# Kernel tuning notes

Hardware: AMD Instinct MI355X
Metric: run time of the kernel (lower is better)

## Reference

```python
import jax, jax.numpy as jnp
import numpy as np

HID = 256; NH = 8; DH = 32; NL = 2
NV = 20000; NT = 50000; NE = 100000; NC = 8; FIN = 64


def setup_inputs() -> dict:
    ks = jax.random.split(jax.random.key(0), 32)
    f = lambda i, sh, s: jax.random.normal(ks[i], sh, dtype=jnp.float32) * s
    return {
        "x_v": f(0, (NV, FIN), 1.0),
        "x_t": f(1, (NT, FIN), 1.0),
        "ei_vt_src": jax.random.randint(ks[2], (NE,), 0, NV),
        "ei_vt_dst": jax.random.randint(ks[3], (NE,), 0, NT),
        "ei_tv_src": jax.random.randint(ks[4], (NE,), 0, NT),
        "ei_tv_dst": jax.random.randint(ks[5], (NE,), 0, NV),
        "ei_tt_src": jax.random.randint(ks[6], (NE,), 0, NT),
        "ei_tt_dst": jax.random.randint(ks[7], (NE,), 0, NT),
        "current": jax.random.randint(ks[8], (NC, 2), 0, NV),
        "W_in_v": f(9, (FIN, HID), 0.05), "b_in_v": jnp.zeros((HID,)),
        "W_in_t": f(10, (FIN, HID), 0.05), "b_in_t": jnp.zeros((HID,)),
        "Wk": f(11, (NL, 2, HID, HID), 0.05), "bk": jnp.zeros((NL, 2, HID)),
        "Wq": f(12, (NL, 2, HID, HID), 0.05), "bq": jnp.zeros((NL, 2, HID)),
        "Wv": f(13, (NL, 2, HID, HID), 0.05), "bv": jnp.zeros((NL, 2, HID)),
        "Wa": f(14, (NL, 2, HID, HID), 0.05), "ba": jnp.zeros((NL, 2, HID)),
        "skip": jnp.zeros((NL, 2)),
        "a_rel": f(15, (NL, 3, NH, DH, DH), 0.1),
        "m_rel": f(16, (NL, 3, NH, DH, DH), 0.1),
        "p_rel": jnp.ones((NL, 3, NH)),
        "Ws1": f(17, (2 * HID, HID), 0.05), "bs1": jnp.zeros((HID,)),
        "Ws2": f(18, (HID, 2), 0.05), "bs2": jnp.zeros((2,)),
    }


def reference(x_v, x_t, ei_vt_src, ei_vt_dst, ei_tv_src, ei_tv_dst,
              ei_tt_src, ei_tt_dst, current,
              W_in_v, b_in_v, W_in_t, b_in_t,
              Wk, bk, Wq, bq, Wv, bv, Wa, ba, skip,
              a_rel, m_rel, p_rel, Ws1, bs1, Ws2, bs2):
    scale = 1.0 / jnp.sqrt(jnp.float32(DH))
    # input projections + relu (lin_dict)
    hv = jax.nn.relu(x_v @ W_in_v + b_in_v)
    ht = jax.nn.relu(x_t @ W_in_t + b_in_t)
    # edge types: (src_type, dst_type, rel_idx, src_idx, dst_idx); 0=vehicle, 1=track
    edges = [(0, 1, 0, ei_vt_src, ei_vt_dst),
             (1, 0, 1, ei_tv_src, ei_tv_dst),
             (1, 1, 2, ei_tt_src, ei_tt_dst)]
    for l in range(NL):
        h = (hv, ht)
        proj = lambda W, b, t: (h[t] @ W[l, t] + b[l, t]).reshape(-1, NH, DH)
        k = (proj(Wk, bk, 0), proj(Wk, bk, 1))
        q = (proj(Wq, bq, 0), proj(Wq, bq, 1))
        v = (proj(Wv, bv, 0), proj(Wv, bv, 1))
        agg = [jnp.zeros((NV, NH, DH), jnp.float32),
               jnp.zeros((NT, NH, DH), jnp.float32)]
        for (st, dt, r, si, di) in edges:
            nd = agg[dt].shape[0]
            ke = jnp.einsum('ehd,hdf->ehf', k[st][si], a_rel[l, r])  # [E,H,D]
            ve = jnp.einsum('ehd,hdf->ehf', v[st][si], m_rel[l, r])  # [E,H,D]
            logit = (q[dt][di] * ke).sum(-1) * p_rel[l, r] * scale    # [E,H]
            m = jax.ops.segment_max(logit, di, num_segments=nd)
            e = jnp.exp(logit - m[di])
            s = jax.ops.segment_sum(e, di, num_segments=nd)
            alpha = e / (s[di] + 1e-16)
            agg[dt] = agg[dt] + jax.ops.segment_sum(alpha[..., None] * ve, di,
                                                    num_segments=nd)
        new = []
        for t in (0, 1):
            o = jax.nn.gelu(agg[t].reshape(-1, HID), approximate=False) @ Wa[l, t] + ba[l, t]
            beta = jax.nn.sigmoid(skip[l, t])
            new.append(beta * o + (1.0 - beta) * h[t])
        hv, ht = new
    # batched Scorer over (current vehicles) x (all tracks); cat([track, vehicle])
    veh = hv[current[:, 0]]                 # [C,HID]
    tpart = ht @ Ws1[:HID]                  # [NT,HID]
    vpart = veh @ Ws1[HID:] + bs1           # [C,HID]
    hmid = jax.nn.relu(tpart[None, :, :] + vpart[:, None, :])  # [C,NT,HID]
    out = hmid @ Ws2 + bs2                  # [C,NT,2]
    return out[..., 0], jax.nn.sigmoid(out[..., 1])
```

## Files before the change

### kernel.cpp

```cpp
#include <hip/hip_runtime.h>
#include <hip/hip_bf16.h>
#include <math.h>

#define HID 256
#define NH 8
#define DH 32
#define NL 2
#define NV 20000
#define NT 50000
#define NE 100000
#define NC 8
#define FIN 64

typedef unsigned short u16;
typedef unsigned int u32;
typedef short s16x8 __attribute__((ext_vector_type(8)));
typedef float f32x4 __attribute__((ext_vector_type(4)));

__device__ __forceinline__ float bf2f(u16 u) { return __uint_as_float(((u32)u) << 16); }
__device__ __forceinline__ u16 f2bf(float f) {
    u32 x = __float_as_uint(f);
    u32 r = ((x >> 16) & 1u) + 0x7fffu;
    return (u16)((x + r) >> 16);
}
__device__ __forceinline__ void up2(u32 u, float& a, float& b) {
    a = __uint_as_float(u << 16);
    b = __uint_as_float(u & 0xffff0000u);
}
__device__ __forceinline__ s16x8 gelu8(s16x8 a) {
    s16x8 r;
#pragma unroll
    for (int i = 0; i < 8; i++) {
        float v = bf2f((u16)a[i]);
        v = 0.5f * v * (1.f + erff(v * 0.70710678118654752f));
        r[i] = (short)f2bf(v);
    }
    return r;
}

__global__ void k_zero_i(int* __restrict__ p, int n) {
    for (int i = blockIdx.x * 256 + threadIdx.x; i < n; i += gridDim.x * 256) p[i] = 0;
}

__global__ void k_hist3(const int* __restrict__ d0, const int* __restrict__ d1, const int* __restrict__ d2,
                        int* __restrict__ cnt3) {
    int r = blockIdx.x >> 9;
    int b = blockIdx.x & 511;
    const int* dst = (r == 0) ? d0 : (r == 1) ? d1 : d2;
    int* cnt = cnt3 + (size_t)r * NT;
    for (int e = b * 256 + threadIdx.x; e < NE; e += 512 * 256)
        atomicAdd(&cnt[dst[e]], 1);
}

__global__ __launch_bounds__(1024) void k_scan3(const int* __restrict__ cnt3,
                                                int* __restrict__ rp0, int* __restrict__ rp1, int* __restrict__ rp2) {
    int r = blockIdx.x;
    const int* cnt = cnt3 + (size_t)r * NT;
    int* rp = (r == 0) ? rp0 : (r == 1) ? rp1 : rp2;
    int n = (r == 1) ? NV : NT;
    __shared__ int wsum[16];
    __shared__ int carry_s;
    int t = threadIdx.x, lane = t & 63, wv = t >> 6;
    if (t == 0) { carry_s = 0; rp[0] = 0; }
    __syncthreads();
    for (int base = 0; base < n; base += 1024) {
        int v = (base + t < n) ? cnt[base + t] : 0;
        int x = v;
#pragma unroll
        for (int off = 1; off < 64; off <<= 1) {
            int y = __shfl_up(x, off, 64);
            if (lane >= off) x += y;
        }
        if (lane == 63) wsum[wv] = x;
        __syncthreads();
        if (wv == 0 && lane < 16) {
            int s = wsum[lane];
#pragma unroll
            for (int off = 1; off < 16; off <<= 1) {
                int y = __shfl_up(s, off, 64);
                if (lane >= off) s += y;
            }
            wsum[lane] = s;
        }
        __syncthreads();
        int prefix = carry_s + (wv > 0 ? wsum[wv - 1] : 0);
        if (base + t < n) rp[base + t + 1] = prefix + x;
        __syncthreads();
        if (t == 0) carry_s += wsum[15];
        __syncthreads();
    }
}

__global__ void k_copy3(const int* __restrict__ rp0, const int* __restrict__ rp1, const int* __restrict__ rp2,
                        int* __restrict__ fill3) {
    int r = blockIdx.x >> 8;
    int b = blockIdx.x & 255;
    const int* rp = (r == 0) ? rp0 : (r == 1) ? rp1 : rp2;
    int n = (r == 1) ? NV : NT;
    int* fill = fill3 + (size_t)r * NT;
    for (int i = b * 256 + threadIdx.x; i < n; i += 256 * 256) fill[i] = rp[i];
}

__global__ void k_scatter3(const int* __restrict__ d0, const int* __restrict__ s0,
                           const int* __restrict__ d1, const int* __restrict__ s1,
                           const int* __restrict__ d2, const int* __restrict__ s2,
                           int* __restrict__ fill3,
                           int* __restrict__ es0, int* __restrict__ es1, int* __restrict__ es2) {
    int r = blockIdx.x >> 9;
    int b = blockIdx.x & 511;
    const int* dst = (r == 0) ? d0 : (r == 1) ? d1 : d2;
    const int* src = (r == 0) ? s0 : (r == 1) ? s1 : s2;
    int* fill = fill3 + (size_t)r * NT;
    int* es = (r == 0) ? es0 : (r == 1) ? es1 : es2;
    for (int e = b * 256 + threadIdx.x; e < NE; e += 512 * 256) {
        int d = dst[e];
        int p = atomicAdd(&fill[d], 1);
        es[p] = src[e];
    }
}

__global__ __launch_bounds__(256) void k_in_proj(const float* __restrict__ X, const float* __restrict__ W,
                          const float* __restrict__ b, u16* __restrict__ Y, int N) {
    const int NPB = 16;
    __shared__ float xs[NPB][FIN];
    int n0 = blockIdx.x * NPB;
    int t = threadIdx.x;
    for (int idx = t; idx < NPB * FIN; idx += 256) {
        int i = idx >> 6, c = idx & 63;
        int n = n0 + i;
        xs[i][c] = (n < N) ? X[(size_t)n * FIN + c] : 0.f;
    }
    __syncthreads();
    float acc[NPB];
#pragma unroll
    for (int i = 0; i < NPB; i++) acc[i] = 0.f;
    for (int c = 0; c < FIN; c++) {
        float w = W[c * HID + t];
#pragma unroll
        for (int i = 0; i < NPB; i++) acc[i] += xs[i][c] * w;
    }
    float bb = b[t];
    for (int i = 0; i < NPB; i++) {
        int n = n0 + i;
        if (n < N) Y[(size_t)n * HID + t] = f2bf(fmaxf(acc[i] + bb, 0.f));
    }
}

__device__ __forceinline__ int swz_idx(int k, int n) {
    int ks = k >> 5, r = k & 31;
    int j = r & 7;
    int l = ((r >> 3) << 4) | (n & 15);
    int nt = n >> 4;
    return ((ks * 16 + nt) * 64 + l) * 8 + j;
}

__global__ __launch_bounds__(256) void k_fuse_w2(
        const float* __restrict__ Wk_, const float* __restrict__ bk_, const float* __restrict__ Rk,
        u16* __restrict__ WswK, float* __restrict__ bkO,
        const float* __restrict__ Wv_, const float* __restrict__ bv_, const float* __restrict__ Rv,
        u16* __restrict__ WswV, float* __restrict__ bvO) {
    int h = blockIdx.x & 7;
    int which = blockIdx.x >> 3;
    const float* W = which ? Wv_ : Wk_;
    const float* b = which ? bv_ : bk_;
    const float* R = which ? Rv : Rk;
    u16* Wsw = which ? WswV : WswK;
    float* bout = which ? bvO : bkO;
    __shared__ float sR[DH * DH];
    int t = threadIdx.x;
    for (int idx = t; idx < DH * DH; idx += 256) sR[idx] = R[h * DH * DH + idx];
    __syncthreads();
    int f = t & 31, c0 = t >> 5;
    for (int c = c0; c < HID; c += 8) {
        float acc = 0.f;
#pragma unroll
        for (int d = 0; d < DH; d++) acc += W[c * HID + h * DH + d] * sR[d * DH + f];
        Wsw[swz_idx(c, h * DH + f)] = f2bf(acc);
    }
    if (t < DH) {
        float acc = 0.f;
#pragma unroll
        for (int d = 0; d < DH; d++) acc += b[h * DH + d] * sR[d * DH + t];
        bout[h * DH + t] = acc;
    }
}

__global__ __launch_bounds__(256) void k_swz_multi(const float* __restrict__ Wq, const float* __restrict__ Wa,
                                                   const float* __restrict__ Ws1, u16* __restrict__ out) {
    int slot = blockIdx.x >> 8;
    int idx = ((blockIdx.x & 255) << 8) | threadIdx.x;
    const float* src = (slot < 4) ? (Wq + (size_t)slot * 65536)
                     : (slot < 8) ? (Wa + (size_t)(slot - 4) * 65536)
                                  : Ws1;
    int j = idx & 7, l = (idx >> 3) & 63, nt = (idx >> 9) & 15, ks = idx >> 13;
    int k = ks * 32 + (l >> 4) * 8 + j;
    int n = nt * 16 + (l & 15);
    out[(size_t)slot * 65536 + idx] = f2bf(src[k * HID + n]);
}

template <int MODE, int GELU>
__global__ __launch_bounds__(256) void k_mm(const u16* __restrict__ X, const u16* __restrict__ Wsw,
                                            const float* __restrict__ bias, void* __restrict__ Y,
                                            const float* __restrict__ skip_, int N) {
    int tid = threadIdx.x;
    int w = tid >> 6, lane = tid & 63;
    int r0 = blockIdx.x * 16;
    int rA = r0 + (lane & 15);
    int koffg = lane >> 4;
    s16x8 a[8];
    if (rA < N) {
        const s16x8* ap = (const s16x8*)(X + (size_t)rA * HID) + koffg;
#pragma unroll
        for (int ks = 0; ks < 8; ks++) a[ks] = ap[ks * 4];
    } else {
#pragma unroll
        for (int ks = 0; ks < 8; ks++) a[ks] = (s16x8){0, 0, 0, 0, 0, 0, 0, 0};
    }
    if (GELU) {
#pragma unroll
        for (int ks = 0; ks < 8; ks++) a[ks] = gelu8(a[ks]);
    }
    f32x4 acc[4];
#pragma unroll
    for (int nt = 0; nt < 4; nt++) acc[nt] = (f32x4){0.f, 0.f, 0.f, 0.f};
    const s16x8* wp = (const s16x8*)Wsw;
#pragma unroll
    for (int ks = 0; ks < 8; ks++) {
        const s16x8* wq = wp + (size_t)ks * 16 * 64 + lane;
#pragma unroll
        for (int nt = 0; nt < 4; nt++) {
            s16x8 b = wq[(w * 4 + nt) * 64];
            acc[nt] = __builtin_amdgcn_mfma_f32_16x16x32_bf16(a[ks], b, acc[nt], 0, 0, 0);
        }
    }
    int colb = lane & 15;
    int rowb = r0 + koffg * 4;
    float beta = 0.f, ombeta = 0.f;
    if (MODE == 2) { beta = 1.f / (1.f + expf(-skip_[0])); ombeta = 1.f - beta; }
#pragma unroll
    for (int nt = 0; nt < 4; nt++) {
        int col = w * 64 + nt * 16 + colb;
        float bb = (MODE == 1 || MODE == 3) ? 0.f : bias[col];
#pragma unroll
        for (int j = 0; j < 4; j++) {
            int row = rowb + j;
            if (row < N) {
                float v = acc[nt][j] + bb;
                if (MODE == 0 || MODE == 3) {
                    ((u16*)Y)[(size_t)row * HID + col] = f2bf(v);
                } else if (MODE == 1) {
                    ((float*)Y)[(size_t)row * HID + col] = v;
                } else {
                    u16* hp = (u16*)Y + (size_t)row * HID + col;
                    *hp = f2bf(beta * v + ombeta * bf2f(*hp));
                }
            }
        }
    }
}

__global__ __launch_bounds__(256) void k_mm_gt(const u16* __restrict__ agg, const u16* __restrict__ WaSw,
                                               const float* __restrict__ ba_, const float* __restrict__ skip_,
                                               const u16* __restrict__ ht_old, const u16* __restrict__ Ws1Sw,
                                               u16* __restrict__ tpart, int N) {
    __shared__ u16 sH[16][264];
    int tid = threadIdx.x;
    int w = tid >> 6, lane = tid & 63;
    int r0 = blockIdx.x * 16;
    int rA = r0 + (lane & 15);
    int koffg = lane >> 4;
    s16x8 a[8];
    {
        const s16x8* ap = (const s16x8*)(agg + (size_t)rA * HID) + koffg;
#pragma unroll
        for (int ks = 0; ks < 8; ks++) a[ks] = gelu8(ap[ks * 4]);
    }
    f32x4 acc[4];
#pragma unroll
    for (int nt = 0; nt < 4; nt++) acc[nt] = (f32x4){0.f, 0.f, 0.f, 0.f};
    const s16x8* wp = (const s16x8*)WaSw;
#pragma unroll
    for (int ks = 0; ks < 8; ks++) {
        const s16x8* wq = wp + (size_t)ks * 16 * 64 + lane;
#pragma unroll
        for (int nt = 0; nt < 4; nt++)
            acc[nt] = __builtin_amdgcn_mfma_f32_16x16x32_bf16(a[ks], wq[(w * 4 + nt) * 64], acc[nt], 0, 0, 0);
    }
    float beta = 1.f / (1.f + expf(-skip_[0])), ombeta = 1.f - beta;
    int colb = lane & 15;
    int rowl = koffg * 4;
#pragma unroll
    for (int nt = 0; nt < 4; nt++) {
        int col = w * 64 + nt * 16 + colb;
        float bb = ba_[col];
#pragma unroll
        for (int j = 0; j < 4; j++) {
            int row = r0 + rowl + j;
            float v = acc[nt][j] + bb;
            float o = beta * v + ombeta * bf2f(ht_old[(size_t)row * HID + col]);
            sH[rowl + j][col] = f2bf(o);
        }
    }
    __syncthreads();
    s16x8 a2[8];
#pragma unroll
    for (int ks = 0; ks < 8; ks++)
        a2[ks] = *(const s16x8*)&sH[lane & 15][ks * 32 + koffg * 8];
#pragma unroll
    for (int nt = 0; nt < 4; nt++) acc[nt] = (f32x4){0.f, 0.f, 0.f, 0.f};
    const s16x8* wp2 = (const s16x8*)Ws1Sw;
#pragma unroll
    for (int ks = 0; ks < 8; ks++) {
        const s16x8* wq = wp2 + (size_t)ks * 16 * 64 + lane;
#pragma unroll
        for (int nt = 0; nt < 4; nt++)
            acc[nt] = __builtin_amdgcn_mfma_f32_16x16x32_bf16(a2[ks], wq[(w * 4 + nt) * 64], acc[nt], 0, 0, 0);
    }
#pragma unroll
    for (int nt = 0; nt < 4; nt++) {
        int col = w * 64 + nt * 16 + colb;
#pragma unroll
        for (int j = 0; j < 4; j++) {
            int row = r0 + rowl + j;
            if (row < N) tpart[(size_t)row * HID + col] = f2bf(acc[nt][j]);
        }
    }
}

__global__ __launch_bounds__(256) void k_mm2(const u16* __restrict__ X,
                                             const u16* __restrict__ W1, const float* __restrict__ b1, u16* __restrict__ Y1,
                                             const u16* __restrict__ W2, const float* __restrict__ b2, u16* __restrict__ Y2,
                                             int N) {
    int tid = threadIdx.x;
    int w = tid >> 6, lane = tid & 63;
    int r0 = blockIdx.x * 16;
    int rA = r0 + (lane & 15);
    int koffg = lane >> 4;
    s16x8 a[8];
    if (rA < N) {
        const s16x8* ap = (const s16x8*)(X + (size_t)rA * HID) + koffg;
#pragma unroll
        for (int ks = 0; ks < 8; ks++) a[ks] = ap[ks * 4];
    } else {
#pragma unroll
        for (int ks = 0; ks < 8; ks++) a[ks] = (s16x8){0, 0, 0, 0, 0, 0, 0, 0};
    }
    int colb = lane & 15;
    int rowb = r0 + koffg * 4;
#pragma unroll
    for (int pass = 0; pass < 2; pass++) {
        const u16* Wsw = pass ? W2 : W1;
        const float* bias = pass ? b2 : b1;
        u16* Y = pass ? Y2 : Y1;
        f32x4 acc[4];
#pragma unroll
        for (int nt = 0; nt < 4; nt++) acc[nt] = (f32x4){0.f, 0.f, 0.f, 0.f};
        const s16x8* wp = (const s16x8*)Wsw;
#pragma unroll
        for (int ks = 0; ks < 8; ks++) {
            const s16x8* wq = wp + (size_t)ks * 16 * 64 + lane;
#pragma unroll
            for (int nt = 0; nt < 4; nt++) {
                s16x8 b = wq[(w * 4 + nt) * 64];
                acc[nt] = __builtin_amdgcn_mfma_f32_16x16x32_bf16(a[ks], b, acc[nt], 0, 0, 0);
            }
        }
#pragma unroll
        for (int nt = 0; nt < 4; nt++) {
            int col = w * 64 + nt * 16 + colb;
            float bb = bias[col];
#pragma unroll
            for (int j = 0; j < 4; j++) {
                int row = rowb + j;
                if (row < N) Y[(size_t)row * HID + col] = f2bf(acc[nt][j] + bb);
            }
        }
    }
}

__global__ __launch_bounds__(256) void k_mm3(const u16* __restrict__ X,
                                             const u16* __restrict__ W0, const float* __restrict__ b0, u16* __restrict__ Y0,
                                             const u16* __restrict__ W1, const float* __restrict__ b1, u16* __restrict__ Y1,
                                             const u16* __restrict__ W2, const float* __restrict__ b2, u16* __restrict__ Y2,
                                             int N) {
    int tid = threadIdx.x;
    int w = tid >> 6, lane = tid & 63;
    int r0 = blockIdx.x * 16;
    int rA = r0 + (lane & 15);
    int koffg = lane >> 4;
    s16x8 a[8];
    if (rA < N) {
        const s16x8* ap = (const s16x8*)(X + (size_t)rA * HID) + koffg;
#pragma unroll
        for (int ks = 0; ks < 8; ks++) a[ks] = ap[ks * 4];
    } else {
#pragma unroll
        for (int ks = 0; ks < 8; ks++) a[ks] = (s16x8){0, 0, 0, 0, 0, 0, 0, 0};
    }
    int colb = lane & 15;
    int rowb = r0 + koffg * 4;
#pragma unroll
    for (int pass = 0; pass < 3; pass++) {
        const u16* Wsw = (pass == 0) ? W0 : (pass == 1) ? W1 : W2;
        const float* bias = (pass == 0) ? b0 : (pass == 1) ? b1 : b2;
        u16* Y = (pass == 0) ? Y0 : (pass == 1) ? Y1 : Y2;
        f32x4 acc[4];
#pragma unroll
        for (int nt = 0; nt < 4; nt++) acc[nt] = (f32x4){0.f, 0.f, 0.f, 0.f};
        const s16x8* wp = (const s16x8*)Wsw;
#pragma unroll
        for (int ks = 0; ks < 8; ks++) {
            const s16x8* wq = wp + (size_t)ks * 16 * 64 + lane;
#pragma unroll
            for (int nt = 0; nt < 4; nt++) {
                s16x8 b = wq[(w * 4 + nt) * 64];
                acc[nt] = __builtin_amdgcn_mfma_f32_16x16x32_bf16(a[ks], b, acc[nt], 0, 0, 0);
            }
        }
#pragma unroll
        for (int nt = 0; nt < 4; nt++) {
            int col = w * 64 + nt * 16 + colb;
            float bb = bias[col];
#pragma unroll
            for (int j = 0; j < 4; j++) {
                int row = rowb + j;
                if (row < N) Y[(size_t)row * HID + col] = f2bf(acc[nt][j] + bb);
            }
        }
    }
}

__device__ __forceinline__ void attn_pass(const u16* __restrict__ kA, const u16* __restrict__ vM,
                                          const int* __restrict__ es, int jb, int je,
                                          float q0, float q1, float q2, float q3, float ph, int lane4,
                                          float& o0, float& o1, float& o2, float& o3) {
    float m = -INFINITY, ss = 0.f, a0 = 0.f, a1 = 0.f, a2 = 0.f, a3 = 0.f;
    uint2 ku0 = {0, 0}, vu0 = {0, 0}, ku1 = {0, 0}, vu1 = {0, 0};
    if (jb < je) {
        int s = es[jb];
        ku0 = *(const uint2*)(kA + (size_t)s * HID + lane4);
        vu0 = *(const uint2*)(vM + (size_t)s * HID + lane4);
    }
    if (jb + 1 < je) {
        int s = es[jb + 1];
        ku1 = *(const uint2*)(kA + (size_t)s * HID + lane4);
        vu1 = *(const uint2*)(vM + (size_t)s * HID + lane4);
    }
    for (int j = jb; j < je; j++) {
        uint2 ku = ku0, vu = vu0;
        ku0 = ku1; vu0 = vu1;
        if (j + 2 < je) {
            int s = es[j + 2];
            ku1 = *(const uint2*)(kA + (size_t)s * HID + lane4);
            vu1 = *(const uint2*)(vM + (size_t)s * HID + lane4);
        }
        float k0, k1, k2, k3; up2(ku.x, k0, k1); up2(ku.y, k2, k3);
        float part = q0 * k0 + q1 * k1 + q2 * k2 + q3 * k3;
        part += __shfl_xor(part, 1, 64);
        part += __shfl_xor(part, 2, 64);
        part += __shfl_xor(part, 4, 64);
        float logit = part * ph;
        float nm = fmaxf(m, logit);
        float corr = expf(m - nm);
        float ee = expf(logit - nm);
        float v0, v1, v2, v3; up2(vu.x, v0, v1); up2(vu.y, v2, v3);
        ss = ss * corr + ee;
        a0 = a0 * corr + ee * v0; a1 = a1 * corr + ee * v1;
        a2 = a2 * corr + ee * v2; a3 = a3 * corr + ee * v3;
        m = nm;
    }
    float inv = 1.f / (ss + 1e-16f);
    o0 += a0 * inv; o1 += a1 * inv; o2 += a2 * inv; o3 += a3 * inv;
}

__global__ __launch_bounds__(256) void k_node_attn(
        const u16* __restrict__ q, const u16* __restrict__ kA, const u16* __restrict__ vM,
        const int* __restrict__ rp, const int* __restrict__ es,
        const float* __restrict__ P, float scale,
        u16* __restrict__ agg, int Nd) {
    int node = blockIdx.x * 4 + (threadIdx.x >> 6);
    if (node >= Nd) return;
    int lane = threadIdx.x & 63;
    float ph = P[lane >> 3] * scale;
    uint2 qu = *(const uint2*)(q + (size_t)node * HID + lane * 4);
    float q0, q1, q2, q3; up2(qu.x, q0, q1); up2(qu.y, q2, q3);
    float o0 = 0.f, o1 = 0.f, o2 = 0.f, o3 = 0.f;
    attn_pass(kA, vM, es, rp[node], rp[node + 1], q0, q1, q2, q3, ph, lane * 4, o0, o1, o2, o3);
    u16* ap = agg + (size_t)node * HID + lane * 4;
    ap[0] = f2bf(o0); ap[1] = f2bf(o1); ap[2] = f2bf(o2); ap[3] = f2bf(o3);
}

__global__ __launch_bounds__(256) void k_node_attn2(
        const u16* __restrict__ q,
        const u16* __restrict__ kA0, const u16* __restrict__ vM0,
        const int* __restrict__ rp0, const int* __restrict__ es0, const float* __restrict__ P0,
        const u16* __restrict__ kA1, const u16* __restrict__ vM1,
        const int* __restrict__ rp1, const int* __restrict__ es1, const float* __restrict__ P1,
        float scale, u16* __restrict__ agg, int Nd) {
    int node = blockIdx.x * 4 + (threadIdx.x >> 6);
    if (node >= Nd) return;
    int lane = threadIdx.x & 63;
    int h = lane >> 3;
    int lane4 = lane * 4;
    float ph0 = P0[h] * scale, ph1 = P1[h] * scale;
    uint2 qu = *(const uint2*)(q + (size_t)node * HID + lane4);
    float q0, q1, q2, q3; up2(qu.x, q0, q1); up2(qu.y, q2, q3);
    float o0 = 0.f, o1 = 0.f, o2 = 0.f, o3 = 0.f;
    attn_pass(kA0, vM0, es0, rp0[node], rp0[node + 1], q0, q1, q2, q3, ph0, lane4, o0, o1, o2, o3);
    attn_pass(kA1, vM1, es1, rp1[node], rp1[node + 1], q0, q1, q2, q3, ph1, lane4, o0, o1, o2, o3);
    u16* ap = agg + (size_t)node * HID + lane4;
    ap[0] = f2bf(o0); ap[1] = f2bf(o1); ap[2] = f2bf(o2); ap[3] = f2bf(o3);
}

__global__ void k_vpart(const u16* __restrict__ hv, const int* __restrict__ current,
                        const float* __restrict__ Ws1, const float* __restrict__ bs1,
                        float* __restrict__ vpart) {
    __shared__ float row[HID];
    int t = threadIdx.x;
    for (int c = 0; c < NC; c++) {
        int n = current[c * 2];
        row[t] = bf2f(hv[(size_t)n * HID + t]);
        __syncthreads();
        float acc = 0.f;
        for (int i = 0; i < HID; i++) acc += row[i] * Ws1[(size_t)(HID + i) * HID + t];
        vpart[c * HID + t] = acc + bs1[t];
        __syncthreads();
    }
}

__global__ __launch_bounds__(256) void k_final(const u16* __restrict__ tpart, const float* __restrict__ vpart,
                        const float* __restrict__ Ws2, const float* __restrict__ bs2,
                        float* __restrict__ out) {
    __shared__ float vp[NC * HID];
    int t = threadIdx.x;
    for (int idx = t; idx < NC * HID; idx += 256) vp[idx] = vpart[idx];
    __syncthreads();
    int lane = t & 63, w = t >> 6;
    float w20[4], w21[4];
#pragma unroll
    for (int i = 0; i < 4; i++) {
        w20[i] = Ws2[(lane + 64 * i) * 2 + 0];
        w21[i] = Ws2[(lane + 64 * i) * 2 + 1];
    }
    float b0 = bs2[0], b1 = bs2[1];
    for (int n = blockIdx.x * 4 + w; n < NT; n += gridDim.x * 4) {
        float tp[4];
#pragma unroll
        for (int i = 0; i < 4; i++) tp[i] = bf2f(tpart[(size_t)n * HID + lane + 64 * i]);
#pragma unroll
        for (int c = 0; c < NC; c++) {
            float a0 = 0.f, a1 = 0.f;
#pragma unroll
            for (int i = 0; i < 4; i++) {
                float hm = fmaxf(tp[i] + vp[c * HID + lane + 64 * i], 0.f);
                a0 += hm * w20[i];
                a1 += hm * w21[i];
            }
#pragma unroll
            for (int off = 32; off >= 1; off >>= 1) {
                a0 += __shfl_xor(a0, off, 64);
                a1 += __shfl_xor(a1, off, 64);
            }
            if (lane == 0) {
                out[(size_t)c * NT + n] = a0 + b0;
                float z = a1 + b1;
                out[(size_t)NC * NT + (size_t)c * NT + n] = 1.f / (1.f + expf(-z));
            }
        }
    }
}

extern "C" void kernel_launch(void* const* d_in, const int* in_sizes, int n_in,
                              void* d_out, int out_size, void* d_ws, size_t ws_size,
                              hipStream_t stream) {
    (void)in_sizes; (void)n_in; (void)out_size;
    const float* x_v    = (const float*)d_in[0];
    const float* x_t    = (const float*)d_in[1];
    const int* ei_vt_s  = (const int*)d_in[2];
    const int* ei_vt_d  = (const int*)d_in[3];
    const int* ei_tv_s  = (const int*)d_in[4];
    const int* ei_tv_d  = (const int*)d_in[5];
    const int* ei_tt_s  = (const int*)d_in[6];
    const int* ei_tt_d  = (const int*)d_in[7];
    const int* current  = (const int*)d_in[8];
    const float* W_in_v = (const float*)d_in[9];
    const float* b_in_v = (const float*)d_in[10];
    const float* W_in_t = (const float*)d_in[11];
    const float* b_in_t = (const float*)d_in[12];
    const float* Wk     = (const float*)d_in[13];
    const float* bk     = (const float*)d_in[14];
    const float* Wq     = (const float*)d_in[15];
    const float* bq     = (const float*)d_in[16];
    const float* Wv     = (const float*)d_in[17];
    const float* bv     = (const float*)d_in[18];
    const float* Wa     = (const float*)d_in[19];
    const float* ba     = (const float*)d_in[20];
    const float* skip   = (const float*)d_in[21];
    const float* a_rel  = (const float*)d_in[22];
    const float* m_rel  = (const float*)d_in[23];
    const float* p_rel  = (const float*)d_in[24];
    const float* Ws1    = (const float*)d_in[25];
    const float* bs1    = (const float*)d_in[26];
    const float* Ws2    = (const float*)d_in[27];
    const float* bs2    = (const float*)d_in[28];

    char* p = (char*)d_ws;
    auto alloc = [&](size_t bytes) -> char* {
        char* r = p;
        p += (bytes + 255) & ~(size_t)255;
        return r;
    };
    u16* hv   = (u16*)alloc((size_t)NV * HID * 2);
    u16* ht   = (u16*)alloc((size_t)NT * HID * 2);
    u16* qb   = (u16*)alloc((size_t)NT * HID * 2);
    u16* qv   = (u16*)alloc((size_t)NV * HID * 2);
    u16* kA   = (u16*)alloc((size_t)NT * HID * 2);
    u16* vM   = (u16*)alloc((size_t)NT * HID * 2);
    u16* kA0  = (u16*)alloc((size_t)NV * HID * 2);
    u16* vM0  = (u16*)alloc((size_t)NV * HID * 2);
    u16* agg  = (u16*)alloc((size_t)NT * HID * 2);
    int* rp_vt = (int*)alloc((size_t)(NT + 1) * 4);
    int* rp_tv = (int*)alloc((size_t)(NV + 1) * 4);
    int* rp_tt = (int*)alloc((size_t)(NT + 1) * 4);
    int* es_vt = (int*)alloc((size_t)NE * 4);
    int* es_tv = (int*)alloc((size_t)NE * 4);
    int* es_tt = (int*)alloc((size_t)NE * 4);
    int* cnt3  = (int*)alloc((size_t)3 * NT * 4);
    int* fill3 = (int*)alloc((size_t)3 * NT * 4);
    float* vp  = (float*)alloc((size_t)NC * HID * 4);
    float* bkF = (float*)alloc(HID * 4);
    float* bvF = (float*)alloc(HID * 4);
    u16*  wswK = (u16*)alloc((size_t)HID * HID * 2);
    u16*  wswV = (u16*)alloc((size_t)HID * HID * 2);
    u16*  wswK2 = (u16*)alloc((size_t)HID * HID * 2);
    u16*  wswV2 = (u16*)alloc((size_t)HID * HID * 2);
    float* bkF2 = (float*)alloc(HID * 4);
    float* bvF2 = (float*)alloc(HID * 4);
    u16*  wswA = (u16*)alloc((size_t)9 * HID * HID * 2);
    if ((size_t)(p - (char*)d_ws) > ws_size) return;

    const float scale = 0.17677669529663687f;

    k_zero_i<<<256, 256, 0, stream>>>(cnt3, 3 * NT);
    k_hist3<<<3 * 512, 256, 0, stream>>>(ei_vt_d, ei_tv_d, ei_tt_d, cnt3);
    k_scan3<<<3, 1024, 0, stream>>>(cnt3, rp_vt, rp_tv, rp_tt);
    k_copy3<<<3 * 256, 256, 0, stream>>>(rp_vt, rp_tv, rp_tt, fill3);
    k_scatter3<<<3 * 512, 256, 0, stream>>>(ei_vt_d, ei_vt_s, ei_tv_d, ei_tv_s, ei_tt_d, ei_tt_s,
                                            fill3, es_vt, es_tv, es_tt);

    k_swz_multi<<<9 * 256, 256, 0, stream>>>(Wq, Wa, Ws1, wswA);

    k_in_proj<<<(NV + 15) / 16, 256, 0, stream>>>(x_v, W_in_v, b_in_v, hv, NV);
    k_in_proj<<<(NT + 15) / 16, 256, 0, stream>>>(x_t, W_in_t, b_in_t, ht, NT);

    const int GV = (NV + 15) / 16, GT = (NT + 15) / 16;

    for (int l = 0; l < NL; l++) {
        const float* Wk0 = Wk + (size_t)(l * 2 + 0) * HID * HID;
        const float* Wk1 = Wk + (size_t)(l * 2 + 1) * HID * HID;
        const float* bk0 = bk + (l * 2 + 0) * HID, *bk1 = bk + (l * 2 + 1) * HID;
        const float* Wv0 = Wv + (size_t)(l * 2 + 0) * HID * HID;
        const float* Wv1 = Wv + (size_t)(l * 2 + 1) * HID * HID;
        const float* bv0 = bv + (l * 2 + 0) * HID, *bv1 = bv + (l * 2 + 1) * HID;
        const float* bq0 = bq + (l * 2 + 0) * HID, *bq1 = bq + (l * 2 + 1) * HID;
        const u16* WqS0 = wswA + (size_t)(l * 2 + 0) * 65536;
        const u16* WqS1 = wswA + (size_t)(l * 2 + 1) * 65536;
        const u16* WaS0 = wswA + (size_t)(4 + l * 2 + 0) * 65536;
        const u16* WaS1 = wswA + (size_t)(4 + l * 2 + 1) * 65536;
        const float* A0 = a_rel + (size_t)(l * 3 + 0) * NH * DH * DH;
        const float* A1 = a_rel + (size_t)(l * 3 + 1) * NH * DH * DH;
        const float* A2 = a_rel + (size_t)(l * 3 + 2) * NH * DH * DH;
        const float* M0 = m_rel + (size_t)(l * 3 + 0) * NH * DH * DH;
        const float* M1 = m_rel + (size_t)(l * 3 + 1) * NH * DH * DH;
        const float* M2 = m_rel + (size_t)(l * 3 + 2) * NH * DH * DH;
        const float* P0 = p_rel + (size_t)(l * 3 + 0) * NH;
        const float* P1 = p_rel + (size_t)(l * 3 + 1) * NH;
        const float* P2 = p_rel + (size_t)(l * 3 + 2) * NH;

        k_fuse_w2<<<2 * NH, 256, 0, stream>>>(Wk0, bk0, A0, wswK, bkF, Wv0, bv0, M0, wswV, bvF);
        k_mm3<<<GV, 256, 0, stream>>>(hv, WqS0, bq0, qv, wswK, bkF, kA0, wswV, bvF, vM0, NV);

        k_fuse_w2<<<2 * NH, 256, 0, stream>>>(Wk1, bk1, A1, wswK, bkF, Wv1, bv1, M1, wswV, bvF);
        k_mm3<<<GT, 256, 0, stream>>>(ht, WqS1, bq1, qb, wswK, bkF, kA, wswV, bvF, vM, NT);

        k_node_attn<<<(NV + 3) / 4, 256, 0, stream>>>(qv, kA, vM, rp_tv, es_tv, P1, scale, agg, NV);

        k_mm<2, 1><<<GV, 256, 0, stream>>>(agg, WaS0, ba + (l * 2 + 0) * HID, hv, skip + (l * 2 + 0), NV);

        k_fuse_w2<<<2 * NH, 256, 0, stream>>>(Wk1, bk1, A2, wswK2, bkF2, Wv1, bv1, M2, wswV2, bvF2);
        k_mm2<<<GT, 256, 0, stream>>>(ht, wswK2, bkF2, kA, wswV2, bvF2, vM, NT);

        k_node_attn2<<<(NT + 3) / 4, 256, 0, stream>>>(qb, kA0, vM0, rp_vt, es_vt, P0,
                                                       kA, vM, rp_tt, es_tt, P2, scale, agg, NT);

        if (l == 0) {
            k_mm<2, 1><<<GT, 256, 0, stream>>>(agg, WaS1, ba + (l * 2 + 1) * HID, ht, skip + (l * 2 + 1), NT);
        } else {
            k_mm_gt<<<GT, 256, 0, stream>>>(agg, WaS1, ba + (l * 2 + 1) * HID, skip + (l * 2 + 1),
                                            ht, wswA + (size_t)8 * 65536, kA, NT);
        }
    }

    k_vpart<<<1, 256, 0, stream>>>(hv, current, Ws1, bs1, vp);
    k_final<<<2048, 256, 0, stream>>>(kA , vp, Ws2, bs2, (float*)d_out);
}
```

Before: 989.6 us.

## Compute last-layer vehicle update only for the current vehicles

```diff
diff --git a/kernel.cpp b/kernel.cpp
--- a/kernel.cpp
+++ b/kernel.cpp
@@ -488,6 +488,40 @@
     attn_pass(kA, vM, es, rp[node], rp[node + 1], q0, q1, q2, q3, ph, lane * 4, o0, o1, o2, o3);
     u16* ap = agg + (size_t)node * HID + lane * 4;
     ap[0] = f2bf(o0); ap[1] = f2bf(o1); ap[2] = f2bf(o2); ap[3] = f2bf(o3);
+}
+
+__global__ __launch_bounds__(256) void k_attn8(
+        const u16* __restrict__ q8, const u16* __restrict__ kA, const u16* __restrict__ vM,
+        const int* __restrict__ rp, const int* __restrict__ es, const int* __restrict__ current,
+        const float* __restrict__ P, float scale, u16* __restrict__ agg8) {
+    int wv = blockIdx.x * 4 + (threadIdx.x >> 6);
+    if (wv >= NC) return;
+    int node = current[wv * 2];
+    int lane = threadIdx.x & 63;
+    int lane4 = lane * 4;
+    float ph = P[lane >> 3] * scale;
+    uint2 qu = *(const uint2*)(q8 + (size_t)wv * HID + lane4);
+    float q0, q1, q2, q3; up2(qu.x, q0, q1); up2(qu.y, q2, q3);
+    float o0 = 0.f, o1 = 0.f, o2 = 0.f, o3 = 0.f;
+    attn_pass(kA, vM, es, rp[node], rp[node + 1], q0, q1, q2, q3, ph, lane4, o0, o1, o2, o3);
+    u16* ap = agg8 + (size_t)wv * HID + lane4;
+    ap[0] = f2bf(o0); ap[1] = f2bf(o1); ap[2] = f2bf(o2); ap[3] = f2bf(o3);
+}
+
+__global__ __launch_bounds__(256) void k_q8(const u16* __restrict__ hv, const int* __restrict__ current,
+                                            const float* __restrict__ Wq_, const float* __restrict__ bq_,
+                                            u16* __restrict__ q8) {
+    __shared__ float row[HID];
+    int t = threadIdx.x;
+    for (int c = 0; c < NC; c++) {
+        int n = current[c * 2];
+        row[t] = bf2f(hv[(size_t)n * HID + t]);
+        __syncthreads();
+        float acc = 0.f;
+        for (int i = 0; i < HID; i++) acc += row[i] * Wq_[i * HID + t];
+        q8[c * HID + t] = f2bf(acc + bq_[t]);
+        __syncthreads();
+    }
 }
 
 __global__ __launch_bounds__(256) void k_node_attn2(
@@ -512,20 +546,47 @@
     ap[0] = f2bf(o0); ap[1] = f2bf(o1); ap[2] = f2bf(o2); ap[3] = f2bf(o3);
 }
 
-__global__ void k_vpart(const u16* __restrict__ hv, const int* __restrict__ current,
-                        const float* __restrict__ Ws1, const float* __restrict__ bs1,
-                        float* __restrict__ vpart) {
-    __shared__ float row[HID];
+__global__ __launch_bounds__(256) void k_vpart_f(
+        const u16* __restrict__ agg8, const float* __restrict__ Wa_, const float* __restrict__ ba_,
+        const float* __restrict__ skip_, const u16* __restrict__ hv, const int* __restrict__ current,
+        const float* __restrict__ Ws1, const float* __restrict__ bs1, float* __restrict__ vpart) {
+    __shared__ float sG[NC][HID];
     int t = threadIdx.x;
+#pragma unroll
+    for (int c = 0; c < NC; c++) {
+        float x = bf2f(agg8[c * HID + t]);
+        sG[c][t] = 0.5f * x * (1.f + erff(x * 0.70710678118654752f));
+    }
+    __syncthreads();
+    float acc[NC];
+#pragma unroll
+    for (int c = 0; c < NC; c++) acc[c] = 0.f;
+    for (int i = 0; i < HID; i++) {
+        float wv_ = Wa_[i * HID + t];
+#pragma unroll
+        for (int c = 0; c < NC; c++) acc[c] += sG[c][i] * wv_;
+    }
+    float beta = 1.f / (1.f + expf(-skip_[0])), ombeta = 1.f - beta;
+    float bb = ba_[t];
+    __syncthreads();
+#pragma unroll
     for (int c = 0; c < NC; c++) {
         int n = current[c * 2];
-        row[t] = bf2f(hv[(size_t)n * HID + t]);
-        __syncthreads();
-        float acc = 0.f;
-        for (int i = 0; i < HID; i++) acc += row[i] * Ws1[(size_t)(HID + i) * HID + t];
-        vpart[c * HID + t] = acc + bs1[t];
-        __syncthreads();
-    }
+        float o = beta * (acc[c] + bb) + ombeta * bf2f(hv[(size_t)n * HID + t]);
+        sG[c][t] = bf2f(f2bf(o));
+    }
+    __syncthreads();
+    float acc2[NC];
+#pragma unroll
+    for (int c = 0; c < NC; c++) acc2[c] = 0.f;
+    for (int i = 0; i < HID; i++) {
+        float w1 = Ws1[(size_t)(HID + i) * HID + t];
+#pragma unroll
+        for (int c = 0; c < NC; c++) acc2[c] += sG[c][i] * w1;
+    }
+    float bs = bs1[t];
+#pragma unroll
+    for (int c = 0; c < NC; c++) vpart[c * HID + t] = acc2[c] + bs;
 }
 
 __global__ __launch_bounds__(256) void k_final(const u16* __restrict__ tpart, const float* __restrict__ vpart,
@@ -628,6 +689,8 @@
     int* cnt3  = (int*)alloc((size_t)3 * NT * 4);
     int* fill3 = (int*)alloc((size_t)3 * NT * 4);
     float* vp  = (float*)alloc((size_t)NC * HID * 4);
+    u16* q8   = (u16*)alloc((size_t)NC * HID * 2);
+    u16* agg8 = (u16*)alloc((size_t)NC * HID * 2);
     float* bkF = (float*)alloc(HID * 4);
     float* bvF = (float*)alloc(HID * 4);
     u16*  wswK = (u16*)alloc((size_t)HID * HID * 2);
@@ -678,14 +741,22 @@
         const float* P2 = p_rel + (size_t)(l * 3 + 2) * NH;
 
         k_fuse_w2<<<2 * NH, 256, 0, stream>>>(Wk0, bk0, A0, wswK, bkF, Wv0, bv0, M0, wswV, bvF);
-        k_mm3<<<GV, 256, 0, stream>>>(hv, WqS0, bq0, qv, wswK, bkF, kA0, wswV, bvF, vM0, NV);
+        if (l == 0) {
+            k_mm3<<<GV, 256, 0, stream>>>(hv, WqS0, bq0, qv, wswK, bkF, kA0, wswV, bvF, vM0, NV);
+        } else {
+            k_mm2<<<GV, 256, 0, stream>>>(hv, wswK, bkF, kA0, wswV, bvF, vM0, NV);
+            k_q8<<<1, 256, 0, stream>>>(hv, current, Wq + (size_t)(l * 2 + 0) * HID * HID, bq0, q8);
+        }
 
         k_fuse_w2<<<2 * NH, 256, 0, stream>>>(Wk1, bk1, A1, wswK, bkF, Wv1, bv1, M1, wswV, bvF);
         k_mm3<<<GT, 256, 0, stream>>>(ht, WqS1, bq1, qb, wswK, bkF, kA, wswV, bvF, vM, NT);
 
-        k_node_attn<<<(NV + 3) / 4, 256, 0, stream>>>(qv, kA, vM, rp_tv, es_tv, P1, scale, agg, NV);
-
-        k_mm<2, 1><<<GV, 256, 0, stream>>>(agg, WaS0, ba + (l * 2 + 0) * HID, hv, skip + (l * 2 + 0), NV);
+        if (l == 0) {
+            k_node_attn<<<(NV + 3) / 4, 256, 0, stream>>>(qv, kA, vM, rp_tv, es_tv, P1, scale, agg, NV);
+            k_mm<2, 1><<<GV, 256, 0, stream>>>(agg, WaS0, ba + (l * 2 + 0) * HID, hv, skip + (l * 2 + 0), NV);
+        } else {
+            k_attn8<<<2, 256, 0, stream>>>(q8, kA, vM, rp_tv, es_tv, current, P1, scale, agg8);
+        }
 
         k_fuse_w2<<<2 * NH, 256, 0, stream>>>(Wk1, bk1, A2, wswK2, bkF2, Wv1, bv1, M2, wswV2, bvF2);
         k_mm2<<<GT, 256, 0, stream>>>(ht, wswK2, bkF2, kA, wswV2, bvF2, vM, NT);
@@ -701,6 +772,7 @@
         }
     }
 
-    k_vpart<<<1, 256, 0, stream>>>(hv, current, Ws1, bs1, vp);
+    k_vpart_f<<<1, 256, 0, stream>>>(agg8, Wa + (size_t)2 * 65536, ba + 2 * HID, skip + 2,
+                                     hv, current, Ws1, bs1, vp);
     k_final<<<2048, 256, 0, stream>>>(kA , vp, Ws2, bs2, (float*)d_out);
 }
```

Result: no change. 976.9 us (-1.3%).
